# Kernel optimization log

Hardware: AMD Instinct MI355X
Metric: run time of the kernel (lower is better)

## Reference

```python
import math
import jax, jax.numpy as jnp
import numpy as np

N_BLOCKS = 8
D_MODEL = 1024
D_FF = 4096
B, T = 4, 2048
EPS = 1e-5


def setup_inputs() -> dict:
    key = jax.random.key(0)
    ks = jax.random.split(key, 8)
    s = 0.02  # small init so deep stack stays numerically sane
    return {
        "x": jax.random.normal(ks[0], (B, T, D_MODEL), jnp.float32),
        "ln1_w": jnp.ones((N_BLOCKS, D_MODEL), jnp.float32),
        "ln1_b": jnp.zeros((N_BLOCKS, D_MODEL), jnp.float32),
        "qkv_w": jax.random.normal(ks[1], (N_BLOCKS, 3 * D_MODEL, D_MODEL), jnp.float32) * s,
        "qkv_b": jnp.zeros((N_BLOCKS, 3 * D_MODEL), jnp.float32),
        "out_w": jax.random.normal(ks[2], (N_BLOCKS, D_MODEL, D_MODEL), jnp.float32) * s,
        "out_b": jnp.zeros((N_BLOCKS, D_MODEL), jnp.float32),
        "ln2_w": jnp.ones((N_BLOCKS, D_MODEL), jnp.float32),
        "ln2_b": jnp.zeros((N_BLOCKS, D_MODEL), jnp.float32),
        "ff0_w": jax.random.normal(ks[3], (N_BLOCKS, D_FF, D_MODEL), jnp.float32) * s,
        "ff0_b": jnp.zeros((N_BLOCKS, D_FF), jnp.float32),
        "ff3_w": jax.random.normal(ks[4], (N_BLOCKS, D_MODEL, D_FF), jnp.float32) * s,
        "ff3_b": jnp.zeros((N_BLOCKS, D_MODEL), jnp.float32),
    }


def _layer_norm(x, w, b):
    mean = jnp.mean(x, axis=-1, keepdims=True)
    var = jnp.mean(jnp.square(x - mean), axis=-1, keepdims=True)
    return (x - mean) / jnp.sqrt(var + EPS) * w + b


def reference(x, ln1_w, ln1_b, qkv_w, qkv_b, out_w, out_b,
              ln2_w, ln2_b, ff0_w, ff0_b, ff3_w, ff3_b):
    Bq, Tq, C = x.shape
    scale = 1.0 / math.sqrt(C)
    mask = jnp.triu(jnp.ones((Tq, Tq), bool), k=1)  # True above diagonal -> masked

    def block(xc, p):
        l1w, l1b, qw, qb, ow, ob, l2w, l2b, f0w, f0b, f3w, f3b = p
        h = _layer_norm(xc, l1w, l1b)
        qkv = h @ qw.T + qb  # [B,T,3C]
        q, k, v = jnp.split(qkv, 3, axis=-1)
        att = jnp.einsum('btc,bsc->bts', q, k) * scale
        att = jnp.where(mask, -jnp.inf, att)
        att = jax.nn.softmax(att, axis=-1)
        out = jnp.einsum('bts,bsc->btc', att, v)
        xc = xc + out @ ow.T + ob
        h2 = _layer_norm(xc, l2w, l2b)
        ff = jax.nn.gelu(h2 @ f0w.T + f0b, approximate=False)
        xc = xc + ff @ f3w.T + f3b
        return xc, None

    params = (ln1_w, ln1_b, qkv_w, qkv_b, out_w, out_b,
              ln2_w, ln2_b, ff0_w, ff0_b, ff3_w, ff3_b)
    x, _ = jax.lax.scan(block, x, params)
    return x
```

## Files before the change

kernel.cpp:

```cpp
#include <hip/hip_runtime.h>
#include <hip/hip_bf16.h>
#include <math.h>


typedef __bf16 bf16;
typedef __bf16 bf16x8 __attribute__((ext_vector_type(8)));
typedef __bf16 bf16x4 __attribute__((ext_vector_type(4)));
typedef float f32x4 __attribute__((ext_vector_type(4)));

#define BM 256
#define BN 256
#define BK 64

__device__ __forceinline__ void async_load16(const void* g, void* l) {
  __builtin_amdgcn_global_load_lds(
      (const __attribute__((address_space(1))) void*)g,
      (__attribute__((address_space(3))) void*)l, 16, 0, 0);
}

__device__ __forceinline__ void barrier_fence() {
  asm volatile("" ::: "memory");
  __builtin_amdgcn_s_barrier();
  asm volatile("" ::: "memory");
}

constexpr int EPI_BF16 = 0;
constexpr int EPI_GELU = 1;
constexpr int EPI_RESID = 2;
constexpr int EPI_F32SCALE = 3;

#define STAGE(S0, S1, LB, HH, JJ, LD)                                \
  do {                                                               \
    const long soff_ = (long)(HH)*128 * (LD) + (long)(JJ)*64;        \
    async_load16((S0) + soff_, (LB) + (HH)*8192);                    \
    async_load16((S1) + soff_, (LB) + (HH)*8192 + 4096);             \
  } while (0)

template <int EPI>
__global__ __launch_bounds__(512, 2) void gemm_bt(
    const bf16* __restrict__ A, const bf16* __restrict__ Bw,
    const float* __restrict__ bias, const float* __restrict__ resid,
    void* __restrict__ Cout, int K, int lda, int ldb, int ldc,
    long batchA, long batchB, long batchC, float alpha,
    int causalSkip, int kLimit) {
  const int nx = gridDim.x;
  const int lin = blockIdx.y * nx + blockIdx.x;
  const int xcd = lin & 7;
  const int tt = lin >> 3;
  const int n_idx = tt % nx;
  const int j_idx = tt / nx;
  const int m0 = (xcd + 8 * j_idx) * BM;
  const int n0 = n_idx * BN;
  if (causalSkip && n0 > m0) return;
  const int bz = blockIdx.z;
  const bf16* Ab = A + (long)bz * batchA;
  const bf16* Bb = Bw + (long)bz * batchB;
  const int kEnd = kLimit ? ((m0 + BM < K) ? (m0 + BM) : K) : K;
  const int nT = kEnd >> 6;

  __shared__ alignas(16) bf16 sm[65536];

  const int tid = threadIdx.x;
  const int wave = tid >> 6;
  const int lane = tid & 63;
  const int wr = wave >> 2;
  const int wc = wave & 3;
  const int l16 = lane & 15;
  const int kq = lane >> 4;

  const int row0 = tid >> 3;
  const int q0 = (tid & 7) ^ ((tid >> 3) & 7);
  const bf16* aS0 = Ab + (long)(m0 + row0) * lda + q0 * 8;
  const bf16* aS1 = aS0 + (long)64 * lda;
  const bf16* bS0 = Bb + (long)(n0 + row0) * ldb + q0 * 8;
  const bf16* bS1 = bS0 + (long)64 * ldb;
  bf16* ldsA = sm + wave * 512;
  bf16* ldsB = sm + 16384 + wave * 512;

  int xk[2];
  xk[0] = ((0 + kq) ^ (l16 & 7)) * 8;
  xk[1] = ((4 + kq) ^ (l16 & 7)) * 8;
  const int aBase = wr * 8192 + l16 * 64;
  const int bBase = 16384 + (wc >> 1) * 8192 + (wc & 1) * 4096 + l16 * 64;

  f32x4 acc[8][4] = {};
  bf16x8 a0[4][2], a1[4][2], b01[2][2], b23[2][2];

  STAGE(aS0, aS1, ldsA, 0, 0, lda);
  STAGE(aS0, aS1, ldsA, 1, 0, lda);
  STAGE(bS0, bS1, ldsB, 0, 0, ldb);
  STAGE(bS0, bS1, ldsB, 1, 0, ldb);
  STAGE(aS0, aS1, ldsA + 32768, 0, 1, lda);
  STAGE(aS0, aS1, ldsA + 32768, 1, 1, lda);
  asm volatile("s_waitcnt vmcnt(4)" ::: "memory");
  barrier_fence();

  for (int t = 0; t < nT; ++t) {
    const int b = t & 1;
    const int aOff = b * 32768 + aBase;
    const int bOff = b * 32768 + bBase;
    bf16* sBn = ldsB + (b ^ 1) * 32768;
    bf16* sAc = ldsA + b * 32768;

#pragma unroll
    for (int mi = 0; mi < 4; ++mi)
#pragma unroll
      for (int ks = 0; ks < 2; ++ks)
        a0[mi][ks] = *(const bf16x8*)(sm + aOff + mi * 1024 + xk[ks]);
#pragma unroll
    for (int ni = 0; ni < 2; ++ni)
#pragma unroll
      for (int ks = 0; ks < 2; ++ks)
        b01[ni][ks] = *(const bf16x8*)(sm + bOff + ni * 1024 + xk[ks]);
    if (t + 1 < nT) STAGE(bS0, bS1, sBn, 0, t + 1, ldb);
    barrier_fence();
    asm volatile("s_waitcnt lgkmcnt(0)" ::: "memory");
    __builtin_amdgcn_s_setprio(1);
#pragma unroll
    for (int mi = 0; mi < 4; ++mi)
#pragma unroll
      for (int ni = 0; ni < 2; ++ni)
#pragma unroll
        for (int ks = 0; ks < 2; ++ks)
          acc[mi][ni] = __builtin_amdgcn_mfma_f32_16x16x32_bf16(
              a0[mi][ks], b01[ni][ks], acc[mi][ni], 0, 0, 0);
    __builtin_amdgcn_s_setprio(0);
    barrier_fence();

#pragma unroll
    for (int mi = 0; mi < 4; ++mi)
#pragma unroll
      for (int ks = 0; ks < 2; ++ks)
        a1[mi][ks] = *(const bf16x8*)(sm + aOff + (mi + 4) * 1024 + xk[ks]);
#pragma unroll
    for (int ni = 0; ni < 2; ++ni)
#pragma unroll
      for (int ks = 0; ks < 2; ++ks)
        b23[ni][ks] = *(const bf16x8*)(sm + bOff + (ni + 2) * 1024 + xk[ks]);
    if (t + 1 < nT) STAGE(bS0, bS1, sBn, 1, t + 1, ldb);
    barrier_fence();
    asm volatile("s_waitcnt lgkmcnt(0)" ::: "memory");
    __builtin_amdgcn_s_setprio(1);
#pragma unroll
    for (int mi = 0; mi < 4; ++mi)
#pragma unroll
      for (int ni = 0; ni < 2; ++ni)
#pragma unroll
        for (int ks = 0; ks < 2; ++ks)
          acc[mi][ni + 2] = __builtin_amdgcn_mfma_f32_16x16x32_bf16(
              a0[mi][ks], b23[ni][ks], acc[mi][ni + 2], 0, 0, 0);
    __builtin_amdgcn_s_setprio(0);
    barrier_fence();

    if (t + 2 < nT) STAGE(aS0, aS1, sAc, 0, t + 2, lda);
    barrier_fence();
    __builtin_amdgcn_s_setprio(1);
#pragma unroll
    for (int mi = 0; mi < 4; ++mi)
#pragma unroll
      for (int ni = 0; ni < 2; ++ni)
#pragma unroll
        for (int ks = 0; ks < 2; ++ks)
          acc[mi + 4][ni + 2] = __builtin_amdgcn_mfma_f32_16x16x32_bf16(
              a1[mi][ks], b23[ni][ks], acc[mi + 4][ni + 2], 0, 0, 0);
    __builtin_amdgcn_s_setprio(0);
    barrier_fence();

    if (t + 2 < nT) {
      STAGE(aS0, aS1, sAc, 1, t + 2, lda);
      asm volatile("s_waitcnt vmcnt(4)" ::: "memory");
    } else if (t + 1 < nT) {
      asm volatile("s_waitcnt vmcnt(0)" ::: "memory");
    }
    barrier_fence();
    __builtin_amdgcn_s_setprio(1);
#pragma unroll
    for (int mi = 0; mi < 4; ++mi)
#pragma unroll
      for (int ni = 0; ni < 2; ++ni)
#pragma unroll
        for (int ks = 0; ks < 2; ++ks)
          acc[mi + 4][ni] = __builtin_amdgcn_mfma_f32_16x16x32_bf16(
              a1[mi][ks], b01[ni][ks], acc[mi + 4][ni], 0, 0, 0);
    __builtin_amdgcn_s_setprio(0);
    barrier_fence();
  }

  const int baseRow = m0 + wr * 128 + (lane >> 4) * 4;
  const int baseCol = n0 + wc * 64 + l16;
#pragma unroll
  for (int ni = 0; ni < 4; ++ni) {
    const int col = baseCol + ni * 16;
    float bv = 0.0f;
    if (EPI != EPI_F32SCALE && bias != nullptr) bv = bias[col];
#pragma unroll
    for (int mi = 0; mi < 8; ++mi) {
      const int rowb = baseRow + mi * 16;
#pragma unroll
      for (int r = 0; r < 4; ++r) {
        const float v = acc[mi][ni][r];
        const long idx = (long)bz * batchC + (long)(rowb + r) * ldc + col;
        if (EPI == EPI_F32SCALE) {
          ((float*)Cout)[idx] = v * alpha;
        } else if (EPI == EPI_RESID) {
          ((float*)Cout)[idx] = resid[idx] + v + bv;
        } else if (EPI == EPI_GELU) {
          const float u = v + bv;
          const float g = 0.5f * u * (1.0f + erff(u * 0.70710678118654752f));
          ((bf16*)Cout)[idx] = (bf16)g;
        } else {
          ((bf16*)Cout)[idx] = (bf16)(v + bv);
        }
      }
    }
  }
}

__global__ __launch_bounds__(256) void ln_kernel(
    const float* __restrict__ x, const float* __restrict__ w,
    const float* __restrict__ b, bf16* __restrict__ out) {
  const int C = 1024;
  const long row = blockIdx.x;
  const int t = threadIdx.x;
  const float4 v = ((const float4*)(x + row * C))[t];
  float s = v.x + v.y + v.z + v.w;
  float sq = v.x * v.x + v.y * v.y + v.z * v.z + v.w * v.w;
#pragma unroll
  for (int o = 1; o < 64; o <<= 1) {
    s += __shfl_xor(s, o, 64);
    sq += __shfl_xor(sq, o, 64);
  }
  __shared__ float rs[4], rq[4];
  const int wv = t >> 6, ln = t & 63;
  if (!ln) { rs[wv] = s; rq[wv] = sq; }
  __syncthreads();
  s = rs[0] + rs[1] + rs[2] + rs[3];
  sq = rq[0] + rq[1] + rq[2] + rq[3];
  const float mean = s * (1.0f / 1024.0f);
  const float var = sq * (1.0f / 1024.0f) - mean * mean;
  const float rstd = rsqrtf(var + 1e-5f);
  const float4 wv4 = ((const float4*)w)[t];
  const float4 bv4 = ((const float4*)b)[t];
  bf16x4 o = {(bf16)((v.x - mean) * rstd * wv4.x + bv4.x),
              (bf16)((v.y - mean) * rstd * wv4.y + bv4.y),
              (bf16)((v.z - mean) * rstd * wv4.z + bv4.z),
              (bf16)((v.w - mean) * rstd * wv4.w + bv4.w)};
  ((bf16x4*)(out + row * C))[t] = o;
}

__global__ __launch_bounds__(256) void softmax_causal(
    const float* __restrict__ S, bf16* __restrict__ P) {
  const int T = 2048;
  const int t = blockIdx.x, b = blockIdx.y;
  const long rowoff = ((long)b * T + t) * (long)T;
  const float* row = S + rowoff;
  bf16* prow = P + rowoff;
  const int L = t + 1;
  const int tid = threadIdx.x;
  float vals[8];
  float mx = -1e30f;
#pragma unroll
  for (int i = 0; i < 8; i++) {
    const int idx = tid + i * 256;
    if (idx < L) {
      vals[i] = row[idx];
      mx = fmaxf(mx, vals[i]);
    } else {
      vals[i] = -1e30f;
    }
  }
#pragma unroll
  for (int o = 1; o < 64; o <<= 1) mx = fmaxf(mx, __shfl_xor(mx, o, 64));
  __shared__ float red[4], red2[4];
  const int wv = tid >> 6, ln = tid & 63;
  if (!ln) red[wv] = mx;
  __syncthreads();
  mx = fmaxf(fmaxf(red[0], red[1]), fmaxf(red[2], red[3]));
  float sum = 0.0f;
#pragma unroll
  for (int i = 0; i < 8; i++) {
    const int idx = tid + i * 256;
    const float e = (idx < L) ? __expf(vals[i] - mx) : 0.0f;
    vals[i] = e;
    sum += e;
  }
#pragma unroll
  for (int o = 1; o < 64; o <<= 1) sum += __shfl_xor(sum, o, 64);
  if (!ln) red2[wv] = sum;
  __syncthreads();
  sum = red2[0] + red2[1] + red2[2] + red2[3];
  const float inv = 1.0f / sum;
#pragma unroll
  for (int i = 0; i < 8; i++) prow[tid + i * 256] = (bf16)(vals[i] * inv);
}

__global__ __launch_bounds__(256) void transpose_v(
    const bf16* __restrict__ qkv, bf16* __restrict__ vt) {
  const int T = 2048, C3 = 3072, C = 1024, COFF = 2048;
  __shared__ bf16 tile[32][33];
  const int b = blockIdx.z;
  const int s0 = blockIdx.x * 32, c0 = blockIdx.y * 32;
  const int tx = threadIdx.x & 31, ty0 = threadIdx.x >> 5;
#pragma unroll
  for (int j = 0; j < 4; j++) {
    const int ty = ty0 + j * 8;
    tile[ty][tx] = qkv[((long)b * T + s0 + ty) * C3 + COFF + c0 + tx];
  }
  __syncthreads();
#pragma unroll
  for (int j = 0; j < 4; j++) {
    const int ty = ty0 + j * 8;
    vt[(long)b * C * T + (long)(c0 + ty) * T + s0 + tx] = tile[tx][ty];
  }
}

__global__ void f2bf_kernel(const float* __restrict__ in,
                            bf16* __restrict__ out, long n4) {
  const long i = (long)blockIdx.x * blockDim.x + threadIdx.x;
  if (i < n4) {
    const float4 v = ((const float4*)in)[i];
    bf16x4 o = {(bf16)v.x, (bf16)v.y, (bf16)v.z, (bf16)v.w};
    ((bf16x4*)out)[i] = o;
  }
}

extern "C" void kernel_launch(void* const* d_in, const int* in_sizes, int n_in,
                              void* d_out, int out_size, void* d_ws,
                              size_t ws_size, hipStream_t stream) {
  const int Bb = 4, T = 2048, C = 1024, FF = 4096, NB = 8;
  const int M = Bb * T;
  const float* x_in = (const float*)d_in[0];
  const float* ln1_w = (const float*)d_in[1];
  const float* ln1_b = (const float*)d_in[2];
  const float* qkv_w = (const float*)d_in[3];
  const float* qkv_b = (const float*)d_in[4];
  const float* out_w = (const float*)d_in[5];
  const float* out_b = (const float*)d_in[6];
  const float* ln2_w = (const float*)d_in[7];
  const float* ln2_b = (const float*)d_in[8];
  const float* ff0_w = (const float*)d_in[9];
  const float* ff0_b = (const float*)d_in[10];
  const float* ff3_w = (const float*)d_in[11];
  const float* ff3_b = (const float*)d_in[12];
  float* x = (float*)d_out;

  char* p = (char*)d_ws;
  auto alloc = [&](size_t bytes) {
    char* r = p;
    p += (bytes + 255) & ~(size_t)255;
    return r;
  };
  bf16* wqkv = (bf16*)alloc((size_t)NB * 3 * C * C * 2);
  bf16* wout = (bf16*)alloc((size_t)NB * C * C * 2);
  bf16* wff0 = (bf16*)alloc((size_t)NB * FF * C * 2);
  bf16* wff3 = (bf16*)alloc((size_t)NB * C * FF * 2);
  bf16* hbuf = (bf16*)alloc((size_t)M * C * 2);
  bf16* qkvb = (bf16*)alloc((size_t)M * 3 * C * 2);
  float* att = (float*)alloc((size_t)Bb * T * T * 4);
  bf16* pbuf = (bf16*)alloc((size_t)Bb * T * T * 2);
  bf16* vt = (bf16*)alloc((size_t)Bb * C * T * 2);
  bf16* aout = (bf16*)alloc((size_t)M * C * 2);
  bf16* ffb = (bf16*)att;

  auto conv = [&](const float* src, bf16* dst, long n) {
    const long n4 = n / 4;
    f2bf_kernel<<<dim3((unsigned)((n4 + 255) / 256)), dim3(256), 0, stream>>>(
        src, dst, n4);
  };
  conv(qkv_w, wqkv, (long)NB * 3 * C * C);
  conv(out_w, wout, (long)NB * C * C);
  conv(ff0_w, wff0, (long)NB * FF * C);
  conv(ff3_w, wff3, (long)NB * C * FF);

  hipMemcpyAsync(x, x_in, (size_t)M * C * 4, hipMemcpyDeviceToDevice, stream);

  const float scale = 1.0f / 32.0f;

  for (int blk = 0; blk < NB; blk++) {
    const bf16* wq = wqkv + (long)blk * 3 * C * C;
    const bf16* wo = wout + (long)blk * C * C;
    const bf16* w0 = wff0 + (long)blk * FF * C;
    const bf16* w3 = wff3 + (long)blk * C * FF;
    const float* l1w = ln1_w + blk * C;
    const float* l1b = ln1_b + blk * C;
    const float* l2w = ln2_w + blk * C;
    const float* l2b = ln2_b + blk * C;
    const float* qb = qkv_b + blk * 3 * C;
    const float* ob = out_b + blk * C;
    const float* f0b = ff0_b + blk * FF;
    const float* f3b = ff3_b + blk * C;

    ln_kernel<<<dim3(M), dim3(256), 0, stream>>>(x, l1w, l1b, hbuf);
    gemm_bt<EPI_BF16><<<dim3(3 * C / BN, M / BM), dim3(512), 0, stream>>>(
        hbuf, wq, qb, nullptr, qkvb, C, C, C, 3 * C, 0, 0, 0, 1.0f, 0, 0);
    gemm_bt<EPI_F32SCALE><<<dim3(T / BN, T / BM, Bb), dim3(512), 0, stream>>>(
        qkvb, qkvb + C, nullptr, nullptr, att, C, 3 * C, 3 * C, T,
        (long)T * 3 * C, (long)T * 3 * C, (long)T * T, scale, 1, 0);
    softmax_causal<<<dim3(T, Bb), dim3(256), 0, stream>>>(att, pbuf);
    transpose_v<<<dim3(T / 32, C / 32, Bb), dim3(256), 0, stream>>>(qkvb, vt);
    gemm_bt<EPI_BF16><<<dim3(C / BN, T / BM, Bb), dim3(512), 0, stream>>>(
        pbuf, vt, nullptr, nullptr, aout, T, T, T, C, (long)T * T, (long)C * T,
        (long)T * C, 1.0f, 0, 1);
    gemm_bt<EPI_RESID><<<dim3(C / BN, M / BM), dim3(512), 0, stream>>>(
        aout, wo, ob, x, x, C, C, C, C, 0, 0, 0, 1.0f, 0, 0);
    ln_kernel<<<dim3(M), dim3(256), 0, stream>>>(x, l2w, l2b, hbuf);
    gemm_bt<EPI_GELU><<<dim3(FF / BN, M / BM), dim3(512), 0, stream>>>(
        hbuf, w0, f0b, nullptr, ffb, C, C, C, FF, 0, 0, 0, 1.0f, 0, 0);
    gemm_bt<EPI_RESID><<<dim3(C / BN, M / BM), dim3(512), 0, stream>>>(
        ffb, w3, f3b, x, x, FF, FF, FF, C, 0, 0, 0, 1.0f, 0, 0);
  }
}
```

Before: 4.383 ms.

## Restructure GEMM main loop into quadrant-interleaved pipeline with inline-asm LDS reads

Rewrites the bf16 GEMM inner loop. Each warp's output tile is now split into 2x2 quadrants (mh, nh) instead of a contiguous 128x64 region, so A and B fragments are reused across two MFMA groups. The prefetch now targets only the next k-tile (t+1) instead of staging A two tiles ahead. LDS reads use explicit ds_read_b128 asm with sched_barrier fences so the compiler cannot reorder loads around the MFMA blocks, and the epilogue is remapped to the new quadrant layout. This aims to cut register pressure and LDS traffic and to overlap global loads with MFMA more tightly. The cost is a shorter prefetch distance and hand-tuned vmcnt counts that are fragile.

```diff
diff --git a/kernel.cpp b/kernel.cpp
--- a/kernel.cpp
+++ b/kernel.cpp
@@ -7,6 +7,7 @@
 typedef __bf16 bf16x8 __attribute__((ext_vector_type(8)));
 typedef __bf16 bf16x4 __attribute__((ext_vector_type(4)));
 typedef float f32x4 __attribute__((ext_vector_type(4)));
+typedef const __attribute__((address_space(3))) bf16* lds_cp;
 
 #define BM 256
 #define BN 256
@@ -16,12 +17,6 @@
   __builtin_amdgcn_global_load_lds(
       (const __attribute__((address_space(1))) void*)g,
       (__attribute__((address_space(3))) void*)l, 16, 0, 0);
-}
-
-__device__ __forceinline__ void barrier_fence() {
-  asm volatile("" ::: "memory");
-  __builtin_amdgcn_s_barrier();
-  asm volatile("" ::: "memory");
 }
 
 constexpr int EPI_BF16 = 0;
@@ -34,6 +29,48 @@
     const long soff_ = (long)(HH)*128 * (LD) + (long)(JJ)*64;        \
     async_load16((S0) + soff_, (LB) + (HH)*8192);                    \
     async_load16((S1) + soff_, (LB) + (HH)*8192 + 4096);             \
+  } while (0)
+
+#define DSR(dst, p) \
+  asm volatile("ds_read_b128 %0, %1" : "=v"(dst) : "v"((lds_cp)(p)))
+
+#define VMW(n) asm volatile("s_waitcnt vmcnt(" #n ")" ::: "memory")
+#define LGKM0                                        \
+  do {                                               \
+    asm volatile("s_waitcnt lgkmcnt(0)" ::: "memory"); \
+    __builtin_amdgcn_sched_barrier(0);               \
+  } while (0)
+
+#define READ_A(MH)                                                   \
+  do {                                                               \
+    const bf16* pa0_ = sm + bufo + (MH)*8192 + aB + xk0;             \
+    const bf16* pa1_ = sm + bufo + (MH)*8192 + aB + xk1;             \
+    DSR(a[0][0], pa0_);        DSR(a[0][1], pa1_);                   \
+    DSR(a[1][0], pa0_ + 1024); DSR(a[1][1], pa1_ + 1024);            \
+    DSR(a[2][0], pa0_ + 2048); DSR(a[2][1], pa1_ + 2048);            \
+    DSR(a[3][0], pa0_ + 3072); DSR(a[3][1], pa1_ + 3072);            \
+  } while (0)
+
+#define READ_B(DST, NH)                                              \
+  do {                                                               \
+    const bf16* pb0_ = sm + bufo + 16384 + (NH)*8192 + bB + xk0;     \
+    const bf16* pb1_ = sm + bufo + 16384 + (NH)*8192 + bB + xk1;     \
+    DSR(DST[0][0], pb0_);        DSR(DST[0][1], pb1_);               \
+    DSR(DST[1][0], pb0_ + 1024); DSR(DST[1][1], pb1_ + 1024);        \
+  } while (0)
+
+#define MFMA16(MH, NH, BMAT)                                               \
+  do {                                                                     \
+    __builtin_amdgcn_s_setprio(1);                                         \
+    _Pragma("unroll") for (int mi = 0; mi < 4; ++mi)                       \
+    _Pragma("unroll") for (int ni = 0; ni < 2; ++ni)                       \
+    _Pragma("unroll") for (int ks = 0; ks < 2; ++ks)                       \
+      acc[(MH)*4 + mi][(NH)*2 + ni] =                                      \
+          __builtin_amdgcn_mfma_f32_16x16x32_bf16(                         \
+              a[mi][ks], BMAT[ni][ks], acc[(MH)*4 + mi][(NH)*2 + ni],      \
+              0, 0, 0);                                                    \
+    __builtin_amdgcn_s_setprio(0);                                         \
+    __builtin_amdgcn_sched_barrier(0);                                     \
   } while (0)
 
 template <int EPI>
@@ -77,139 +114,98 @@
   bf16* ldsA = sm + wave * 512;
   bf16* ldsB = sm + 16384 + wave * 512;
 
-  int xk[2];
-  xk[0] = ((0 + kq) ^ (l16 & 7)) * 8;
-  xk[1] = ((4 + kq) ^ (l16 & 7)) * 8;
-  const int aBase = wr * 8192 + l16 * 64;
-  const int bBase = 16384 + (wc >> 1) * 8192 + (wc & 1) * 4096 + l16 * 64;
+  const int xk0 = (kq ^ (l16 & 7)) * 8;
+  const int xk1 = ((4 + kq) ^ (l16 & 7)) * 8;
+  const int aB = (wr * 64 + l16) * 64;
+  const int bB = (wc * 32 + l16) * 64;
 
   f32x4 acc[8][4] = {};
-  bf16x8 a0[4][2], a1[4][2], b01[2][2], b23[2][2];
+  bf16x8 a[4][2], b0[2][2], b1[2][2];
 
   STAGE(aS0, aS1, ldsA, 0, 0, lda);
-  STAGE(aS0, aS1, ldsA, 1, 0, lda);
   STAGE(bS0, bS1, ldsB, 0, 0, ldb);
   STAGE(bS0, bS1, ldsB, 1, 0, ldb);
-  STAGE(aS0, aS1, ldsA + 32768, 0, 1, lda);
-  STAGE(aS0, aS1, ldsA + 32768, 1, 1, lda);
-  asm volatile("s_waitcnt vmcnt(4)" ::: "memory");
-  barrier_fence();
+  STAGE(aS0, aS1, ldsA, 1, 0, lda);
+  VMW(4);
+  __builtin_amdgcn_s_barrier();
 
   for (int t = 0; t < nT; ++t) {
-    const int b = t & 1;
-    const int aOff = b * 32768 + aBase;
-    const int bOff = b * 32768 + bBase;
-    bf16* sBn = ldsB + (b ^ 1) * 32768;
-    bf16* sAc = ldsA + b * 32768;
-
-#pragma unroll
-    for (int mi = 0; mi < 4; ++mi)
-#pragma unroll
-      for (int ks = 0; ks < 2; ++ks)
-        a0[mi][ks] = *(const bf16x8*)(sm + aOff + mi * 1024 + xk[ks]);
-#pragma unroll
-    for (int ni = 0; ni < 2; ++ni)
-#pragma unroll
-      for (int ks = 0; ks < 2; ++ks)
-        b01[ni][ks] = *(const bf16x8*)(sm + bOff + ni * 1024 + xk[ks]);
-    if (t + 1 < nT) STAGE(bS0, bS1, sBn, 0, t + 1, ldb);
-    barrier_fence();
-    asm volatile("s_waitcnt lgkmcnt(0)" ::: "memory");
-    __builtin_amdgcn_s_setprio(1);
-#pragma unroll
-    for (int mi = 0; mi < 4; ++mi)
-#pragma unroll
-      for (int ni = 0; ni < 2; ++ni)
-#pragma unroll
-        for (int ks = 0; ks < 2; ++ks)
-          acc[mi][ni] = __builtin_amdgcn_mfma_f32_16x16x32_bf16(
-              a0[mi][ks], b01[ni][ks], acc[mi][ni], 0, 0, 0);
-    __builtin_amdgcn_s_setprio(0);
-    barrier_fence();
-
-#pragma unroll
-    for (int mi = 0; mi < 4; ++mi)
-#pragma unroll
-      for (int ks = 0; ks < 2; ++ks)
-        a1[mi][ks] = *(const bf16x8*)(sm + aOff + (mi + 4) * 1024 + xk[ks]);
-#pragma unroll
-    for (int ni = 0; ni < 2; ++ni)
-#pragma unroll
-      for (int ks = 0; ks < 2; ++ks)
-        b23[ni][ks] = *(const bf16x8*)(sm + bOff + (ni + 2) * 1024 + xk[ks]);
-    if (t + 1 < nT) STAGE(bS0, bS1, sBn, 1, t + 1, ldb);
-    barrier_fence();
-    asm volatile("s_waitcnt lgkmcnt(0)" ::: "memory");
-    __builtin_amdgcn_s_setprio(1);
-#pragma unroll
-    for (int mi = 0; mi < 4; ++mi)
-#pragma unroll
-      for (int ni = 0; ni < 2; ++ni)
-#pragma unroll
-        for (int ks = 0; ks < 2; ++ks)
-          acc[mi][ni + 2] = __builtin_amdgcn_mfma_f32_16x16x32_bf16(
-              a0[mi][ks], b23[ni][ks], acc[mi][ni + 2], 0, 0, 0);
-    __builtin_amdgcn_s_setprio(0);
-    barrier_fence();
-
-    if (t + 2 < nT) STAGE(aS0, aS1, sAc, 0, t + 2, lda);
-    barrier_fence();
-    __builtin_amdgcn_s_setprio(1);
-#pragma unroll
-    for (int mi = 0; mi < 4; ++mi)
-#pragma unroll
-      for (int ni = 0; ni < 2; ++ni)
-#pragma unroll
-        for (int ks = 0; ks < 2; ++ks)
-          acc[mi + 4][ni + 2] = __builtin_amdgcn_mfma_f32_16x16x32_bf16(
-              a1[mi][ks], b23[ni][ks], acc[mi + 4][ni + 2], 0, 0, 0);
-    __builtin_amdgcn_s_setprio(0);
-    barrier_fence();
-
-    if (t + 2 < nT) {
-      STAGE(aS0, aS1, sAc, 1, t + 2, lda);
-      asm volatile("s_waitcnt vmcnt(4)" ::: "memory");
-    } else if (t + 1 < nT) {
-      asm volatile("s_waitcnt vmcnt(0)" ::: "memory");
+    const unsigned bufo = (t & 1) ? 32768u : 0u;
+    bf16* sAn = ldsA + (((t + 1) & 1) ? 32768 : 0);
+    bf16* sBn = ldsB + (((t + 1) & 1) ? 32768 : 0);
+    const bool pf = (t + 1 < nT);
+
+    READ_A(0);
+    READ_B(b0, 0);
+    if (pf) {
+      STAGE(aS0, aS1, sAn, 0, t + 1, lda);
+      VMW(4);
+    } else {
+      VMW(2);
     }
-    barrier_fence();
-    __builtin_amdgcn_s_setprio(1);
-#pragma unroll
-    for (int mi = 0; mi < 4; ++mi)
-#pragma unroll
-      for (int ni = 0; ni < 2; ++ni)
-#pragma unroll
-        for (int ks = 0; ks < 2; ++ks)
-          acc[mi + 4][ni] = __builtin_amdgcn_mfma_f32_16x16x32_bf16(
-              a1[mi][ks], b01[ni][ks], acc[mi + 4][ni], 0, 0, 0);
-    __builtin_amdgcn_s_setprio(0);
-    barrier_fence();
-  }
-
-  const int baseRow = m0 + wr * 128 + (lane >> 4) * 4;
-  const int baseCol = n0 + wc * 64 + l16;
-#pragma unroll
-  for (int ni = 0; ni < 4; ++ni) {
-    const int col = baseCol + ni * 16;
-    float bv = 0.0f;
-    if (EPI != EPI_F32SCALE && bias != nullptr) bv = bias[col];
-#pragma unroll
-    for (int mi = 0; mi < 8; ++mi) {
-      const int rowb = baseRow + mi * 16;
-#pragma unroll
-      for (int r = 0; r < 4; ++r) {
-        const float v = acc[mi][ni][r];
-        const long idx = (long)bz * batchC + (long)(rowb + r) * ldc + col;
-        if (EPI == EPI_F32SCALE) {
-          ((float*)Cout)[idx] = v * alpha;
-        } else if (EPI == EPI_RESID) {
-          ((float*)Cout)[idx] = resid[idx] + v + bv;
-        } else if (EPI == EPI_GELU) {
-          const float u = v + bv;
-          const float g = 0.5f * u * (1.0f + erff(u * 0.70710678118654752f));
-          ((bf16*)Cout)[idx] = (bf16)g;
-        } else {
-          ((bf16*)Cout)[idx] = (bf16)(v + bv);
+    __builtin_amdgcn_s_barrier();
+    LGKM0;
+    MFMA16(0, 0, b0);
+    __builtin_amdgcn_s_barrier();
+
+    READ_B(b1, 1);
+    if (pf) {
+      STAGE(bS0, bS1, sBn, 0, t + 1, ldb);
+      VMW(4);
+    } else {
+      VMW(0);
+    }
+    __builtin_amdgcn_s_barrier();
+    LGKM0;
+    MFMA16(0, 1, b1);
+    __builtin_amdgcn_s_barrier();
+
+    READ_A(1);
+    if (pf) STAGE(bS0, bS1, sBn, 1, t + 1, ldb);
+    __builtin_amdgcn_s_barrier();
+    LGKM0;
+    MFMA16(1, 1, b1);
+    __builtin_amdgcn_s_barrier();
+
+    if (pf) {
+      STAGE(aS0, aS1, sAn, 1, t + 1, lda);
+      VMW(4);
+    }
+    __builtin_amdgcn_s_barrier();
+    MFMA16(1, 0, b0);
+    __builtin_amdgcn_s_barrier();
+  }
+
+  const int laneRow = (lane >> 4) * 4;
+#pragma unroll
+  for (int nh = 0; nh < 2; ++nh) {
+#pragma unroll
+    for (int ni = 0; ni < 2; ++ni) {
+      const int col = n0 + nh * 128 + wc * 32 + ni * 16 + l16;
+      float bv = 0.0f;
+      if (EPI != EPI_F32SCALE && bias != nullptr) bv = bias[col];
+#pragma unroll
+      for (int mh = 0; mh < 2; ++mh) {
+#pragma unroll
+        for (int mi = 0; mi < 4; ++mi) {
+          const int rowb = m0 + mh * 128 + wr * 64 + mi * 16 + laneRow;
+          const f32x4 v4 = acc[mh * 4 + mi][nh * 2 + ni];
+#pragma unroll
+          for (int r = 0; r < 4; ++r) {
+            const float v = v4[r];
+            const long idx = (long)bz * batchC + (long)(rowb + r) * ldc + col;
+            if (EPI == EPI_F32SCALE) {
+              ((float*)Cout)[idx] = v * alpha;
+            } else if (EPI == EPI_RESID) {
+              ((float*)Cout)[idx] = resid[idx] + v + bv;
+            } else if (EPI == EPI_GELU) {
+              const float u = v + bv;
+              const float g = 0.5f * u * (1.0f + erff(u * 0.70710678118654752f));
+              ((bf16*)Cout)[idx] = (bf16)g;
+            } else {
+              ((bf16*)Cout)[idx] = (bf16)(v + bv);
+            }
+          }
         }
       }
     }
```

Measured after the change: 4.267 ms. -2.6%, faster.
